# Optimization experiments

Hardware: AMD Instinct MI355X
Metric: run time of the kernel (lower is better)

The kernel has to match this reference:

```python
import jax, jax.numpy as jnp
import numpy as np

N, E, G = 20000, 160000, 32          # nodes, edges, graphs in batch
F_IN, H, P, C = 67, 2048, 1024, 18   # in_feat, hidden_feat, fc2 width, n_classifier
EPS = 1e-5
SLOPE = 0.01  # leaky_relu default negative slope


def setup_inputs() -> dict:
    key = jax.random.key(0)
    ks = jax.random.split(key, 24)
    w = lambda k, shape: (jax.random.normal(k, shape, jnp.float32) * 0.02)
    return {
        "h": jax.random.normal(ks[0], (N, F_IN), jnp.float32),
        "src": jax.random.randint(ks[1], (E,), 0, N),
        "dst": jax.random.randint(ks[2], (E,), 0, N),
        "gids": jnp.sort(jax.random.randint(ks[3], (N,), 0, G)),
        # SAGEConv layers: fc_self, fc_neigh (no per-fc bias), shared bias
        "ws1": w(ks[4], (F_IN, H)), "wn1": w(ks[5], (F_IN, H)), "b1": jnp.zeros((H,), jnp.float32),
        "ws2": w(ks[6], (H, H)),    "wn2": w(ks[7], (H, H)),    "b2": jnp.zeros((H,), jnp.float32),
        "ws3": w(ks[8], (H, H)),    "wn3": w(ks[9], (H, H)),    "b3": jnp.zeros((H,), jnp.float32),
        # batch norms (gamma, beta)
        "g1": jnp.ones((H,), jnp.float32), "be1": jnp.zeros((H,), jnp.float32),
        "g2": jnp.ones((H,), jnp.float32), "be2": jnp.zeros((H,), jnp.float32),
        "g3": jnp.ones((H,), jnp.float32), "be3": jnp.zeros((H,), jnp.float32),
        # MLP head
        "fw1": w(ks[10], (H, H)), "fb1": jnp.zeros((H,), jnp.float32),
        "fw2": w(ks[11], (H, P)), "fb2": jnp.zeros((P,), jnp.float32),
        "fw3": w(ks[12], (P, C)), "fb3": jnp.zeros((C,), jnp.float32),
    }


def _leaky(x):
    return jnp.where(x >= 0, x, SLOPE * x)


def _sage(x, src, dst, w_self, w_neigh, b):
    # DGL SAGEConv 'mean': mean of neighbor (src) features into dst, then linears.
    nsum = jax.ops.segment_sum(x[src], dst, num_segments=N)            # [N, F]
    deg = jax.ops.segment_sum(jnp.ones((E,), x.dtype), dst, num_segments=N)
    neigh = nsum / jnp.maximum(deg, 1.0)[:, None]                      # 0 for isolated
    return x @ w_self + neigh @ w_neigh + b


def _bn(x, gamma, beta):
    m = x.mean(0)
    v = x.var(0)
    return (x - m) * jax.lax.rsqrt(v + EPS) * gamma + beta


def reference(h, src, dst, gids,
              ws1, wn1, b1, g1, be1,
              ws2, wn2, b2, g2, be2,
              ws3, wn3, b3, g3, be3,
              fw1, fb1, fw2, fb2, fw3, fb3):
    x = _leaky(_bn(_sage(h, src, dst, ws1, wn1, b1), g1, be1))
    x = _leaky(_bn(_sage(x, src, dst, ws2, wn2, b2), g2, be2))
    x = _leaky(_bn(_sage(x, src, dst, ws3, wn3, b3), g3, be3))
    # mean pooling per graph
    gsum = jax.ops.segment_sum(x, gids, num_segments=G)                # [G, H]
    cnt = jax.ops.segment_sum(jnp.ones((N,), x.dtype), gids, num_segments=G)
    hg = gsum / jnp.maximum(cnt, 1.0)[:, None]
    # dropouts are identity in eval
    y = _leaky(hg @ fw1 + fb1)
    y = _leaky(y @ fw2 + fb2)
    return y @ fw3 + fb3
```

## Files before the change

### kernel.cpp

```cpp
#include <hip/hip_runtime.h>

typedef unsigned short u16;
typedef __attribute__((ext_vector_type(4))) float f32x4;
typedef __attribute__((ext_vector_type(8))) __bf16 bf16x8;
typedef __attribute__((ext_vector_type(8))) short s16x8;
typedef __attribute__((ext_vector_type(4))) u16 u16x4;

#define N_NODES 20000
#define N_EDGES 160000
#define N_GRAPH 32
#define F_IN 67
#define HID 2048
#define PW 1024
#define NCLS 18
#define MPAD2 20224
#define K1 192

__device__ __forceinline__ float bf2f(u16 u) {
    unsigned v = ((unsigned)u) << 16;
    float f; __builtin_memcpy(&f, &v, 4); return f;
}
__device__ __forceinline__ u16 f2bf(float f) {
    unsigned u; __builtin_memcpy(&u, &f, 4);
    u = (u + 0x7FFF + ((u >> 16) & 1)) >> 16;
    return (u16)u;
}
__device__ __forceinline__ int imax(int a, int b) { return a > b ? a : b; }

__device__ __forceinline__ void ld16(const u16* gptr, u16* lptr) {
    __builtin_amdgcn_global_load_lds(
        (const __attribute__((address_space(1))) unsigned int*)gptr,
        (__attribute__((address_space(3))) unsigned int*)lptr,
        16, 0, 0);
}

__global__ void k_hist(const int* __restrict__ dst, int* __restrict__ cnt) {
    int e = blockIdx.x * 256 + threadIdx.x;
    if (e < N_EDGES) atomicAdd(&cnt[dst[e]], 1);
}

__global__ void k_scan(const int* __restrict__ cnt, int* __restrict__ rowptr) {
    __shared__ int part[256];
    int t = threadIdx.x;
    const int per = (N_NODES + 255) / 256;
    int base = t * per;
    int s = 0;
    for (int i = 0; i < per; i++) { int idx = base + i; if (idx < N_NODES) s += cnt[idx]; }
    part[t] = s; __syncthreads();
    for (int off = 1; off < 256; off <<= 1) {
        int v = (t >= off) ? part[t - off] : 0;
        __syncthreads();
        part[t] += v;
        __syncthreads();
    }
    int running = (t == 0) ? 0 : part[t - 1];
    for (int i = 0; i < per; i++) {
        int idx = base + i;
        if (idx < N_NODES) { rowptr[idx] = running; running += cnt[idx]; }
    }
    if (t == 255) rowptr[N_NODES] = running;
}

__global__ void k_scatter(const int* __restrict__ src, const int* __restrict__ dst,
                          const int* __restrict__ rowptr, int* __restrict__ cursor,
                          int* __restrict__ csr) {
    int e = blockIdx.x * 256 + threadIdx.x;
    if (e < N_EDGES) {
        int d = dst[e];
        int p = atomicAdd(&cursor[d], 1);
        csr[rowptr[d] + p] = src[e];
    }
}

__global__ void k_w1t(const float* __restrict__ ws1, const float* __restrict__ wn1,
                      u16* __restrict__ w1t) {
    int n = blockIdx.x, t = threadIdx.x;
    float v = 0.f;
    if (t < F_IN) v = ws1[(size_t)t * HID + n];
    else if (t < 2 * F_IN) v = wn1[(size_t)(t - F_IN) * HID + n];
    w1t[(size_t)n * K1 + t] = f2bf(v);
}

__global__ void k_transpose2(const float* __restrict__ s0, const float* __restrict__ s1,
                             u16* __restrict__ dst) {
    __shared__ float tile[32][33];
    const float* src = blockIdx.z ? s1 : s0;
    int colofs = blockIdx.z ? HID : 0;
    int bx = blockIdx.x * 32, by = blockIdx.y * 32;
    int tx = threadIdx.x, ty = threadIdx.y;
#pragma unroll
    for (int i = 0; i < 32; i += 8)
        tile[ty + i][tx] = src[(size_t)(by + ty + i) * HID + bx + tx];
    __syncthreads();
#pragma unroll
    for (int i = 0; i < 32; i += 8)
        dst[(size_t)(bx + ty + i) * (2 * HID) + colofs + by + tx] = f2bf(tile[tx][ty + i]);
}

__global__ void k_agg1(const float* __restrict__ h, const int* __restrict__ rowptr,
                       const int* __restrict__ csr, u16* __restrict__ acat) {
    int n = blockIdx.x, t = threadIdx.x;
    if (t < F_IN) {
        acat[(size_t)n * K1 + t] = f2bf(h[(size_t)n * F_IN + t]);
    } else if (t < 2 * F_IN) {
        int c = t - F_IN;
        int e0 = rowptr[n], e1 = rowptr[n + 1];
        float a = 0.f;
        for (int e = e0; e < e1; e++) a += h[(size_t)csr[e] * F_IN + c];
        acat[(size_t)n * K1 + F_IN + c] = f2bf(a / (float)imax(e1 - e0, 1));
    }
}

__global__ __launch_bounds__(256)
void k_aggbn(const u16* __restrict__ x,
             const float* __restrict__ ssum, const float* __restrict__ ssq,
             const float* __restrict__ gma, const float* __restrict__ bta,
             const int* __restrict__ rowptr, const int* __restrict__ csr,
             u16* __restrict__ self_out, u16* __restrict__ neigh_out) {
    int n = blockIdx.x, t = threadIdx.x;
    int col = t * 8;
    float a[8], d[8];
#pragma unroll
    for (int j = 0; j < 8; ++j) {
        float m = ssum[col + j] * (1.0f / N_NODES);
        float var = ssq[col + j] * (1.0f / N_NODES) - m * m;
        a[j] = gma[col + j] * rsqrtf(var + 1e-5f);
        d[j] = bta[col + j] - m * a[j];
    }
    s16x8 vs = *(const s16x8*)&x[(size_t)n * HID + col];
    s16x8 so;
#pragma unroll
    for (int j = 0; j < 8; ++j) {
        float f = bf2f((u16)vs[j]) * a[j] + d[j];
        f = fmaxf(f, 0.01f * f);
        so[j] = (short)f2bf(f);
    }
    *(s16x8*)&self_out[(size_t)n * HID + col] = so;
    int e0 = rowptr[n], e1 = rowptr[n + 1];
    float acc[8] = {0, 0, 0, 0, 0, 0, 0, 0};
    for (int e = e0; e < e1; ++e) {
        int s = csr[e];
        s16x8 v = *(const s16x8*)&x[(size_t)s * HID + col];
#pragma unroll
        for (int j = 0; j < 8; ++j) {
            float f = bf2f((u16)v[j]) * a[j] + d[j];
            acc[j] += fmaxf(f, 0.01f * f);
        }
    }
    float inv = 1.0f / (float)imax(e1 - e0, 1);
    s16x8 o;
#pragma unroll
    for (int j = 0; j < 8; ++j) o[j] = (short)f2bf(acc[j] * inv);
    *(s16x8*)&neigh_out[(size_t)n * HID + col] = o;
}

#define VM4 asm volatile("s_waitcnt vmcnt(4)" ::: "memory")
#define VM2 asm volatile("s_waitcnt vmcnt(2)" ::: "memory")
#define VM0 asm volatile("s_waitcnt vmcnt(0)" ::: "memory")

#define STAGE_A(H) { const u16* as_; int ktl_;                                      \
    if (kt1 < kskt) { as_ = A0; ktl_ = kt1; } else { as_ = A1; ktl_ = kt1 - kskt; } \
    size_t ko_ = (size_t)ktl_ * 64 + swe;                                           \
    ld16(as_ + (row0 + 0 * 128 + (H) * 64 + r8) * (size_t)lda + ko_,                \
         LA + dbo + ((H) * 128 + 0 * 64 + r8) * 64 + ld8);                          \
    ld16(as_ + (row0 + 1 * 128 + (H) * 64 + r8) * (size_t)lda + ko_,                \
         LA + dbo + ((H) * 128 + 1 * 64 + r8) * 64 + ld8); }

#define STAGE_B(H) { size_t ko_ = (size_t)kt1 * 64 + swe;                           \
    ld16(WT + ((size_t)col0 + ((r8 >> 5)) * 64 + (H) * 32 + (r8 & 31)) * (size_t)ldb + ko_,\
         LB + dbo + ((H) * 128 + 0 * 64 + r8) * 64 + ld8);                          \
    ld16(WT + ((size_t)col0 + (2 + (r8 >> 5)) * 64 + (H) * 32 + (r8 & 31)) * (size_t)ldb + ko_,\
         LB + dbo + ((H) * 128 + 1 * 64 + r8) * 64 + ld8); }

#define RD_A(QM) {                                                                  \
    _Pragma("unroll") for (int f = 0; f < 4; ++f)                                   \
      _Pragma("unroll") for (int kk = 0; kk < 2; ++kk)                              \
        af[f][kk] = *(const bf16x8*)(bA + (QM) * 16384 + (wm * 64 + f * 16 + lr) * 128 \
                                     + ((kk * 64 + lg * 16) ^ rxor)); }

#define RD_B(DST, QN) {                                                             \
    _Pragma("unroll") for (int n = 0; n < 2; ++n)                                   \
      _Pragma("unroll") for (int kk = 0; kk < 2; ++kk)                              \
        DST[n][kk] = *(const bf16x8*)(bB + (QN) * 16384 + (wn * 32 + n * 16 + lr) * 128 \
                                     + ((kk * 64 + lg * 16) ^ rxor)); }

#define SYNC_MM(QM, QN, BW) {                                                       \
    __builtin_amdgcn_s_barrier();                                                   \
    __builtin_amdgcn_s_setprio(1);                                                  \
    _Pragma("unroll") for (int kk = 0; kk < 2; ++kk)                                \
      _Pragma("unroll") for (int f = 0; f < 4; ++f)                                 \
        _Pragma("unroll") for (int n = 0; n < 2; ++n)                               \
          acc[(QM) * 4 + f][(QN) * 2 + n] = __builtin_amdgcn_mfma_f32_16x16x32_bf16(\
              BW[n][kk], af[f][kk], acc[(QM) * 4 + f][(QN) * 2 + n], 0, 0, 0);      \
    __builtin_amdgcn_s_setprio(0); }

__global__ __launch_bounds__(512, 2)
void k_gemm256(const u16* __restrict__ A0, const u16* __restrict__ A1,
               const u16* __restrict__ WT, u16* __restrict__ C,
               float* __restrict__ ssum, float* __restrict__ ssq,
               int nkt, int kskt, int lda, int ldb) {
    __shared__ u16 LA[2 * 256 * 64];
    __shared__ u16 LB[2 * 256 * 64];
    const int tid = threadIdx.x;
    const int lane = tid & 63;
    const int wave = tid >> 6;
    const int wm = wave >> 2, wn = wave & 3;
    const int lr = lane & 15, lg = lane >> 4;
    const int rxor = (lr & 7) << 4;

    const int g = (blockIdx.x & 7) * 79 + (blockIdx.x >> 3);
    const size_t row0 = (size_t)(g >> 3) * 256;
    const int col0 = (g & 7) * 256;

    const int r8 = tid >> 3;
    const int ld8 = (tid & 7) * 8;
    const int swe = ((ld8 * 2) ^ ((r8 & 7) << 4)) >> 1;

    f32x4 acc[8][4];
#pragma unroll
    for (int i = 0; i < 8; i++)
#pragma unroll
        for (int j = 0; j < 4; j++) acc[i][j] = f32x4{0.f, 0.f, 0.f, 0.f};

    {
        const int kt1 = 0; const int dbo = 0;
        STAGE_A(0) STAGE_B(0) STAGE_B(1) STAGE_A(1)
    }
    VM0;
    __builtin_amdgcn_s_barrier();

    bf16x8 af[4][2], bw[2][2], bw2[2][2];

    for (int t = 0; t < nkt - 1; ++t) {
        const char* bA = (const char*)LA + (t & 1) * 32768;
        const char* bB = (const char*)LB + (t & 1) * 32768;
        const int kt1 = t + 1;
        const int dbo = ((t + 1) & 1) * 16384;
        RD_A(0) RD_B(bw, 0) STAGE_A(0) VM4; SYNC_MM(0, 0, bw)
        RD_B(bw2, 1) STAGE_B(0) VM4; SYNC_MM(0, 1, bw2)
        RD_A(1) STAGE_B(1) SYNC_MM(1, 1, bw2)
        RD_B(bw, 0) STAGE_A(1) VM4; SYNC_MM(1, 0, bw)
    }
    {
        const char* bA = (const char*)LA + ((nkt - 1) & 1) * 32768;
        const char* bB = (const char*)LB + ((nkt - 1) & 1) * 32768;
        RD_A(0) RD_B(bw, 0) VM2; SYNC_MM(0, 0, bw)
        RD_B(bw2, 1) VM0; SYNC_MM(0, 1, bw2)
        RD_A(1) SYNC_MM(1, 1, bw2)
        RD_B(bw, 0) SYNC_MM(1, 0, bw)
    }

#pragma unroll
    for (int f = 0; f < 8; ++f) {
        size_t m = row0 + wm * 128 + f * 16 + lr;
#pragma unroll
        for (int n = 0; n < 4; ++n) {
            int cb = col0 + wn * 64 + n * 16 + lg * 4;
            u16x4 o;
#pragma unroll
            for (int rg = 0; rg < 4; ++rg) o[rg] = f2bf(acc[f][n][rg]);
            *(u16x4*)&C[m * HID + cb] = o;
        }
    }
#pragma unroll
    for (int n = 0; n < 4; ++n) {
#pragma unroll
        for (int rg = 0; rg < 4; ++rg) {
            float s = 0.f, s2 = 0.f;
#pragma unroll
            for (int f = 0; f < 8; ++f) { float v = acc[f][n][rg]; s += v; s2 += v * v; }
#pragma unroll
            for (int mk = 1; mk < 16; mk <<= 1) {
                s += __shfl_xor(s, mk, 64);
                s2 += __shfl_xor(s2, mk, 64);
            }
            if (lr == 0) {
                int cb = col0 + wn * 64 + n * 16 + lg * 4 + rg;
                atomicAdd(&ssum[cb], s);
                atomicAdd(&ssq[cb], s2);
            }
        }
    }
}

__global__ void k_bounds(const int* __restrict__ gids, int* __restrict__ gstart) {
    int t = threadIdx.x;
    if (t > N_GRAPH) return;
    int lo = 0, hi = N_NODES;
    while (lo < hi) { int mid = (lo + hi) >> 1; if (gids[mid] < t) lo = mid + 1; else hi = mid; }
    gstart[t] = lo;
}

__global__ void k_poolbn(const u16* __restrict__ x,
                         const float* __restrict__ ssum, const float* __restrict__ ssq,
                         const float* __restrict__ gma, const float* __restrict__ bta,
                         const int* __restrict__ gstart, float* __restrict__ hg) {
    int g = blockIdx.x;
    int col = blockIdx.y * 256 + threadIdx.x;
    float m = ssum[col] * (1.0f / N_NODES);
    float var = ssq[col] * (1.0f / N_NODES) - m * m;
    float a = gma[col] * rsqrtf(var + 1e-5f);
    float d = bta[col] - m * a;
    int r0 = gstart[g], r1 = gstart[g + 1];
    float s = 0.f;
    for (int r = r0; r < r1; r++) {
        float f = bf2f(x[(size_t)r * HID + col]) * a + d;
        s += fmaxf(f, 0.01f * f);
    }
    hg[(size_t)g * HID + col] = s / (float)imax(r1 - r0, 1);
}

__global__ __launch_bounds__(256)
void k_mlp_part(const float* __restrict__ X, const float* __restrict__ W,
                float* __restrict__ Yp, int K, int Nc) {
    __shared__ float xs[32 * 256];
    int t = threadIdx.x;
    int kc = blockIdx.y;
    int n = blockIdx.x * 64 + (t & 63);
    int mg = t >> 6;
#pragma unroll
    for (int l = 0; l < 32; ++l) {
        int e = l * 256 + t;
        xs[e] = X[(size_t)(e >> 8) * K + kc * 256 + (e & 255)];
    }
    __syncthreads();
    float acc[8] = {};
    for (int k = 0; k < 256; ++k) {
        float wv = W[(size_t)(kc * 256 + k) * Nc + n];
#pragma unroll
        for (int i = 0; i < 8; ++i) acc[i] += xs[(mg * 8 + i) * 256 + k] * wv;
    }
#pragma unroll
    for (int i = 0; i < 8; ++i)
        Yp[(size_t)(kc * 32 + mg * 8 + i) * Nc + n] = acc[i];
}

__global__ void k_mlp_red(const float* __restrict__ Yp, const float* __restrict__ bias,
                          float* __restrict__ Y, int Nc, int leaky) {
    int idx = blockIdx.x * 256 + threadIdx.x;
    int n = idx % Nc;
    float s = 0.f;
#pragma unroll
    for (int kc = 0; kc < 8; ++kc) s += Yp[(size_t)kc * 32 * Nc + idx];
    float v = s + bias[n];
    if (leaky) v = v > 0.f ? v : 0.01f * v;
    Y[idx] = v;
}

__global__ void k_fc3(const float* __restrict__ y2, const float* __restrict__ fw3,
                      const float* __restrict__ fb3, float* __restrict__ out) {
    __shared__ float red[8][32];
    int m = blockIdx.x, t = threadIdx.x;
    int ch = t >> 5, c = t & 31;
    float s = 0.f;
    if (c < NCLS) {
        for (int j = 0; j < 128; ++j) {
            int k = ch * 128 + j;
            s += y2[(size_t)m * PW + k] * fw3[(size_t)k * NCLS + c];
        }
    }
    red[ch][c] = s;
    __syncthreads();
    if (t < NCLS) {
        float a = 0.f;
#pragma unroll
        for (int c2 = 0; c2 < 8; ++c2) a += red[c2][t];
        out[m * NCLS + t] = a + fb3[t];
    }
}

extern "C" void kernel_launch(void* const* d_in, const int* in_sizes, int n_in,
                              void* d_out, int out_size, void* d_ws, size_t ws_size,
                              hipStream_t stream) {
    const float* h   = (const float*)d_in[0];
    const int* src   = (const int*)d_in[1];
    const int* dst   = (const int*)d_in[2];
    const int* gids  = (const int*)d_in[3];
    const float* ws1 = (const float*)d_in[4];
    const float* wn1 = (const float*)d_in[5];
    const float* ws2 = (const float*)d_in[7];
    const float* wn2 = (const float*)d_in[8];
    const float* ws3 = (const float*)d_in[10];
    const float* wn3 = (const float*)d_in[11];
    const float* g1  = (const float*)d_in[13];
    const float* be1 = (const float*)d_in[14];
    const float* g2  = (const float*)d_in[15];
    const float* be2 = (const float*)d_in[16];
    const float* g3  = (const float*)d_in[17];
    const float* be3 = (const float*)d_in[18];
    const float* fw1 = (const float*)d_in[19];
    const float* fb1 = (const float*)d_in[20];
    const float* fw2 = (const float*)d_in[21];
    const float* fb2 = (const float*)d_in[22];
    const float* fw3 = (const float*)d_in[23];
    const float* fb3 = (const float*)d_in[24];
    float* out = (float*)d_out;
    (void)in_sizes; (void)n_in; (void)out_size;

    char* base = (char*)d_ws;
    size_t off = 0;
    auto alloc = [&](size_t b) -> char* {
        char* p = base + off;
        off += (b + 255) & ~(size_t)255;
        return p;
    };
    u16* BUF0 = (u16*)alloc((size_t)MPAD2 * HID * 2);
    u16* BUF1 = (u16*)alloc((size_t)MPAD2 * HID * 2);
    u16* BUF2 = (u16*)alloc((size_t)MPAD2 * HID * 2);
    u16* WT   = (u16*)alloc((size_t)HID * 2 * HID * 2);
    int* cnt    = (int*)alloc(N_NODES * 4);
    int* rowptr = (int*)alloc((N_NODES + 1) * 4);
    int* cursor = (int*)alloc(N_NODES * 4);
    int* csr    = (int*)alloc(N_EDGES * 4);
    float* ssum = (float*)alloc(HID * 4);
    float* ssq  = (float*)alloc(HID * 4);
    int* gstart = (int*)alloc(64 * 4);
    float* hg = (float*)alloc((size_t)N_GRAPH * HID * 4);
    float* y1 = (float*)alloc((size_t)N_GRAPH * HID * 4);
    float* y2 = (float*)alloc((size_t)N_GRAPH * PW * 4);
    u16* ACAT = (u16*)((char*)BUF2);
    u16* W1T  = (u16*)((char*)BUF2 + (size_t)MPAD2 * K1 * 2);
    float* Yp = (float*)((char*)BUF2);

    if (off > ws_size) return;

    hipMemsetAsync(cnt, 0, N_NODES * 4, stream);
    hipMemsetAsync(cursor, 0, N_NODES * 4, stream);
    hipMemsetAsync(ACAT, 0, (size_t)MPAD2 * K1 * 2, stream);
    hipMemsetAsync(BUF1 + (size_t)N_NODES * HID, 0, (size_t)(MPAD2 - N_NODES) * HID * 2, stream);
    hipMemsetAsync(BUF2 + (size_t)N_NODES * HID, 0, (size_t)(MPAD2 - N_NODES) * HID * 2, stream);

    k_hist<<<(N_EDGES + 255) / 256, 256, 0, stream>>>(dst, cnt);
    k_scan<<<1, 256, 0, stream>>>(cnt, rowptr);
    k_scatter<<<(N_EDGES + 255) / 256, 256, 0, stream>>>(src, dst, rowptr, cursor, csr);

    k_w1t<<<HID, K1, 0, stream>>>(ws1, wn1, W1T);
    k_agg1<<<N_NODES, 192, 0, stream>>>(h, rowptr, csr, ACAT);

    dim3 tb(32, 8);
    hipMemsetAsync(ssum, 0, 2 * HID * 4, stream);
    k_gemm256<<<632, 512, 0, stream>>>(ACAT, ACAT, W1T, BUF0, ssum, ssq, 3, 3, K1, K1);
    k_aggbn<<<N_NODES, 256, 0, stream>>>(BUF0, ssum, ssq, g1, be1, rowptr, csr, BUF1, BUF2);
    k_transpose2<<<dim3(64, 64, 2), tb, 0, stream>>>(ws2, wn2, WT);
    hipMemsetAsync(ssum, 0, 2 * HID * 4, stream);
    k_gemm256<<<632, 512, 0, stream>>>(BUF1, BUF2, WT, BUF0, ssum, ssq, 64, 32, HID, 2 * HID);
    k_aggbn<<<N_NODES, 256, 0, stream>>>(BUF0, ssum, ssq, g2, be2, rowptr, csr, BUF1, BUF2);
    k_transpose2<<<dim3(64, 64, 2), tb, 0, stream>>>(ws3, wn3, WT);
    hipMemsetAsync(ssum, 0, 2 * HID * 4, stream);
    k_gemm256<<<632, 512, 0, stream>>>(BUF1, BUF2, WT, BUF0, ssum, ssq, 64, 32, HID, 2 * HID);
    k_bounds<<<1, 64, 0, stream>>>(gids, gstart);
    k_poolbn<<<dim3(N_GRAPH, HID / 256), 256, 0, stream>>>(BUF0, ssum, ssq, g3, be3, gstart, hg);
    k_mlp_part<<<dim3(HID / 64, 8), 256, 0, stream>>>(hg, fw1, Yp, HID, HID);
    k_mlp_red<<<(N_GRAPH * HID) / 256, 256, 0, stream>>>(Yp, fb1, y1, HID, 1);
    k_mlp_part<<<dim3(PW / 64, 8), 256, 0, stream>>>(y1, fw2, Yp, HID, PW);
    k_mlp_red<<<(N_GRAPH * PW) / 256, 256, 0, stream>>>(Yp, fb2, y2, PW, 1);
    k_fc3<<<N_GRAPH, 256, 0, stream>>>(y2, fw3, fb3, out);
}
```

Baseline: 1.351 ms.

## Halve GEMM K-tile to 32 and restructure LDS staging and barriers

The 256x256 GEMM kernel now stages a K-slice of 32 instead of 64 per iteration. This halves LDS use (32 KB instead of 64 KB) and removes the launch_bounds occupancy hint. The global-to-LDS mapping, swizzle and wave-to-tile mapping are rewritten: each wave now covers interleaved 64-row and 32-column sub-blocks, and barriers are split from the MFMA groups. The aim is to cut the LDS footprint and let the pipeline overlap better, at the cost of twice as many K iterations and barriers.

Result: slower. 1.479 ms (+9.5%).

```diff
diff --git a/kernel.cpp b/kernel.cpp
--- a/kernel.cpp
+++ b/kernel.cpp
@@ -154,67 +154,60 @@
     *(s16x8*)&neigh_out[(size_t)n * HID + col] = o;
 }
 
-#define VM4 asm volatile("s_waitcnt vmcnt(4)" ::: "memory")
 #define VM2 asm volatile("s_waitcnt vmcnt(2)" ::: "memory")
 #define VM0 asm volatile("s_waitcnt vmcnt(0)" ::: "memory")
-
-#define STAGE_A(H) { const u16* as_; int ktl_;                                      \
+#define BAR __builtin_amdgcn_s_barrier();
+
+#define STAGE_A() { const u16* as_; int ktl_;                                       \
     if (kt1 < kskt) { as_ = A0; ktl_ = kt1; } else { as_ = A1; ktl_ = kt1 - kskt; } \
-    size_t ko_ = (size_t)ktl_ * 64 + swe;                                           \
-    ld16(as_ + (row0 + 0 * 128 + (H) * 64 + r8) * (size_t)lda + ko_,                \
-         LA + dbo + ((H) * 128 + 0 * 64 + r8) * 64 + ld8);                          \
-    ld16(as_ + (row0 + 1 * 128 + (H) * 64 + r8) * (size_t)lda + ko_,                \
-         LA + dbo + ((H) * 128 + 1 * 64 + r8) * 64 + ld8); }
-
-#define STAGE_B(H) { size_t ko_ = (size_t)kt1 * 64 + swe;                           \
-    ld16(WT + ((size_t)col0 + ((r8 >> 5)) * 64 + (H) * 32 + (r8 & 31)) * (size_t)ldb + ko_,\
-         LB + dbo + ((H) * 128 + 0 * 64 + r8) * 64 + ld8);                          \
-    ld16(WT + ((size_t)col0 + (2 + (r8 >> 5)) * 64 + (H) * 32 + (r8 & 31)) * (size_t)ldb + ko_,\
-         LB + dbo + ((H) * 128 + 1 * 64 + r8) * 64 + ld8); }
-
-#define RD_A(QM) {                                                                  \
+    size_t kb_ = (size_t)ktl_ * 32 + ksl;                                           \
+    ld16(as_ + (row0 + grow0) * (size_t)lda + kb_, LA + dbo + ldsoff);              \
+    ld16(as_ + (row0 + grow0 + 128) * (size_t)lda + kb_, LA + dbo + 4096 + ldsoff); }
+
+#define STAGE_B() { size_t kb_ = (size_t)kt1 * 32 + ksl;                            \
+    ld16(WT + (size_t)(col0 + grow0) * ldb + kb_, LB + dbo + ldsoff);               \
+    ld16(WT + (size_t)(col0 + grow0 + 128) * ldb + kb_, LB + dbo + 4096 + ldsoff); }
+
+#define RD_A(QM) { _Pragma("unroll") for (int f = 0; f < 4; ++f)                    \
+    af[f] = *(const bf16x8*)(bA + ((QM) * 64 + aq + f * 8) * 128 + hbx); }
+
+#define RD_B(DST, QN) { _Pragma("unroll") for (int n = 0; n < 2; ++n)               \
+    DST[n] = *(const bf16x8*)(bB + ((QN) * 64 + bq + n * 8) * 128 + hbx); }
+
+#define MM8(QM, QN, BW) {                                                           \
+    __builtin_amdgcn_s_setprio(1);                                                  \
     _Pragma("unroll") for (int f = 0; f < 4; ++f)                                   \
-      _Pragma("unroll") for (int kk = 0; kk < 2; ++kk)                              \
-        af[f][kk] = *(const bf16x8*)(bA + (QM) * 16384 + (wm * 64 + f * 16 + lr) * 128 \
-                                     + ((kk * 64 + lg * 16) ^ rxor)); }
-
-#define RD_B(DST, QN) {                                                             \
-    _Pragma("unroll") for (int n = 0; n < 2; ++n)                                   \
-      _Pragma("unroll") for (int kk = 0; kk < 2; ++kk)                              \
-        DST[n][kk] = *(const bf16x8*)(bB + (QN) * 16384 + (wn * 32 + n * 16 + lr) * 128 \
-                                     + ((kk * 64 + lg * 16) ^ rxor)); }
-
-#define SYNC_MM(QM, QN, BW) {                                                       \
-    __builtin_amdgcn_s_barrier();                                                   \
-    __builtin_amdgcn_s_setprio(1);                                                  \
-    _Pragma("unroll") for (int kk = 0; kk < 2; ++kk)                                \
-      _Pragma("unroll") for (int f = 0; f < 4; ++f)                                 \
-        _Pragma("unroll") for (int n = 0; n < 2; ++n)                               \
-          acc[(QM) * 4 + f][(QN) * 2 + n] = __builtin_amdgcn_mfma_f32_16x16x32_bf16(\
-              BW[n][kk], af[f][kk], acc[(QM) * 4 + f][(QN) * 2 + n], 0, 0, 0);      \
+      _Pragma("unroll") for (int n = 0; n < 2; ++n)                                 \
+        acc[(QM) * 4 + f][(QN) * 2 + n] = __builtin_amdgcn_mfma_f32_16x16x32_bf16(  \
+            BW[n], af[f], acc[(QM) * 4 + f][(QN) * 2 + n], 0, 0, 0);                \
     __builtin_amdgcn_s_setprio(0); }
 
-__global__ __launch_bounds__(512, 2)
+__global__ __launch_bounds__(512)
 void k_gemm256(const u16* __restrict__ A0, const u16* __restrict__ A1,
                const u16* __restrict__ WT, u16* __restrict__ C,
                float* __restrict__ ssum, float* __restrict__ ssq,
                int nkt, int kskt, int lda, int ldb) {
-    __shared__ u16 LA[2 * 256 * 64];
-    __shared__ u16 LB[2 * 256 * 64];
+    __shared__ u16 LA[2 * 128 * 64];
+    __shared__ u16 LB[2 * 128 * 64];
     const int tid = threadIdx.x;
     const int lane = tid & 63;
     const int wave = tid >> 6;
     const int wm = wave >> 2, wn = wave & 3;
     const int lr = lane & 15, lg = lane >> 4;
-    const int rxor = (lr & 7) << 4;
 
     const int g = (blockIdx.x & 7) * 79 + (blockIdx.x >> 3);
     const size_t row0 = (size_t)(g >> 3) * 256;
     const int col0 = (g & 7) * 256;
 
-    const int r8 = tid >> 3;
-    const int ld8 = (tid & 7) * 8;
-    const int swe = ((ld8 * 2) ^ ((r8 & 7) << 4)) >> 1;
+    const int q0 = tid >> 3;
+    const int lg16 = ((tid & 7) * 16) ^ ((q0 & 7) << 4);
+    const int grow0 = 2 * q0 + (lg16 >> 6);
+    const int ksl = ((lg16 >> 4) & 3) * 8;
+    const int ldsoff = tid * 8;
+
+    const int aq = wm * 32 + (lr >> 1);
+    const int bq = wn * 16 + (lr >> 1);
+    const int hbx = (((lane & 1) * 64 + lg * 16) ^ (((lr >> 1) & 7) << 4));
 
     f32x4 acc[8][4];
 #pragma unroll
@@ -224,58 +217,58 @@
 
     {
         const int kt1 = 0; const int dbo = 0;
-        STAGE_A(0) STAGE_B(0) STAGE_B(1) STAGE_A(1)
+        STAGE_A() STAGE_B()
     }
     VM0;
-    __builtin_amdgcn_s_barrier();
-
-    bf16x8 af[4][2], bw[2][2], bw2[2][2];
+    BAR
+
+    bf16x8 af[4], bw[2], bw2[2];
 
     for (int t = 0; t < nkt - 1; ++t) {
-        const char* bA = (const char*)LA + (t & 1) * 32768;
-        const char* bB = (const char*)LB + (t & 1) * 32768;
+        const char* bA = (const char*)LA + (t & 1) * 16384;
+        const char* bB = (const char*)LB + (t & 1) * 16384;
         const int kt1 = t + 1;
-        const int dbo = ((t + 1) & 1) * 16384;
-        RD_A(0) RD_B(bw, 0) STAGE_A(0) VM4; SYNC_MM(0, 0, bw)
-        RD_B(bw2, 1) STAGE_B(0) VM4; SYNC_MM(0, 1, bw2)
-        RD_A(1) STAGE_B(1) SYNC_MM(1, 1, bw2)
-        RD_B(bw, 0) STAGE_A(1) VM4; SYNC_MM(1, 0, bw)
+        const int dbo = ((t + 1) & 1) * 8192;
+        RD_A(0) RD_B(bw, 0) STAGE_A() VM2; BAR MM8(0, 0, bw)
+        RD_B(bw2, 1) STAGE_B() BAR MM8(0, 1, bw2)
+        RD_A(1) BAR MM8(1, 1, bw2)
+        MM8(1, 0, bw)
     }
     {
-        const char* bA = (const char*)LA + ((nkt - 1) & 1) * 32768;
-        const char* bB = (const char*)LB + ((nkt - 1) & 1) * 32768;
-        RD_A(0) RD_B(bw, 0) VM2; SYNC_MM(0, 0, bw)
-        RD_B(bw2, 1) VM0; SYNC_MM(0, 1, bw2)
-        RD_A(1) SYNC_MM(1, 1, bw2)
-        RD_B(bw, 0) SYNC_MM(1, 0, bw)
-    }
-
-#pragma unroll
-    for (int f = 0; f < 8; ++f) {
-        size_t m = row0 + wm * 128 + f * 16 + lr;
-#pragma unroll
-        for (int n = 0; n < 4; ++n) {
-            int cb = col0 + wn * 64 + n * 16 + lg * 4;
+        const char* bA = (const char*)LA + ((nkt - 1) & 1) * 16384;
+        const char* bB = (const char*)LB + ((nkt - 1) & 1) * 16384;
+        RD_A(0) RD_B(bw, 0) VM0; BAR MM8(0, 0, bw)
+        RD_B(bw2, 1) BAR MM8(0, 1, bw2)
+        RD_A(1) BAR MM8(1, 1, bw2)
+        MM8(1, 0, bw)
+    }
+
+#pragma unroll
+    for (int i = 0; i < 8; ++i) {
+        size_t m = row0 + (i >> 2) * 128 + wm * 64 + (i & 3) * 16 + lr;
+#pragma unroll
+        for (int j = 0; j < 4; ++j) {
+            int cb = col0 + (j >> 1) * 128 + wn * 32 + (j & 1) * 16 + lg * 4;
             u16x4 o;
 #pragma unroll
-            for (int rg = 0; rg < 4; ++rg) o[rg] = f2bf(acc[f][n][rg]);
+            for (int rg = 0; rg < 4; ++rg) o[rg] = f2bf(acc[i][j][rg]);
             *(u16x4*)&C[m * HID + cb] = o;
         }
     }
 #pragma unroll
-    for (int n = 0; n < 4; ++n) {
+    for (int j = 0; j < 4; ++j) {
 #pragma unroll
         for (int rg = 0; rg < 4; ++rg) {
             float s = 0.f, s2 = 0.f;
 #pragma unroll
-            for (int f = 0; f < 8; ++f) { float v = acc[f][n][rg]; s += v; s2 += v * v; }
+            for (int i = 0; i < 8; ++i) { float v = acc[i][j][rg]; s += v; s2 += v * v; }
 #pragma unroll
             for (int mk = 1; mk < 16; mk <<= 1) {
                 s += __shfl_xor(s, mk, 64);
                 s2 += __shfl_xor(s2, mk, 64);
             }
             if (lr == 0) {
-                int cb = col0 + wn * 64 + n * 16 + lg * 4 + rg;
+                int cb = col0 + (j >> 1) * 128 + wn * 32 + (j & 1) * 16 + lg * 4 + rg;
                 atomicAdd(&ssum[cb], s);
                 atomicAdd(&ssq[cb], s2);
             }
@@ -439,15 +432,15 @@
 
     dim3 tb(32, 8);
     hipMemsetAsync(ssum, 0, 2 * HID * 4, stream);
-    k_gemm256<<<632, 512, 0, stream>>>(ACAT, ACAT, W1T, BUF0, ssum, ssq, 3, 3, K1, K1);
+    k_gemm256<<<632, 512, 0, stream>>>(ACAT, ACAT, W1T, BUF0, ssum, ssq, 6, 6, K1, K1);
     k_aggbn<<<N_NODES, 256, 0, stream>>>(BUF0, ssum, ssq, g1, be1, rowptr, csr, BUF1, BUF2);
     k_transpose2<<<dim3(64, 64, 2), tb, 0, stream>>>(ws2, wn2, WT);
     hipMemsetAsync(ssum, 0, 2 * HID * 4, stream);
-    k_gemm256<<<632, 512, 0, stream>>>(BUF1, BUF2, WT, BUF0, ssum, ssq, 64, 32, HID, 2 * HID);
+    k_gemm256<<<632, 512, 0, stream>>>(BUF1, BUF2, WT, BUF0, ssum, ssq, 128, 64, HID, 2 * HID);
     k_aggbn<<<N_NODES, 256, 0, stream>>>(BUF0, ssum, ssq, g2, be2, rowptr, csr, BUF1, BUF2);
     k_transpose2<<<dim3(64, 64, 2), tb, 0, stream>>>(ws3, wn3, WT);
     hipMemsetAsync(ssum, 0, 2 * HID * 4, stream);
-    k_gemm256<<<632, 512, 0, stream>>>(BUF1, BUF2, WT, BUF0, ssum, ssq, 64, 32, HID, 2 * HID);
+    k_gemm256<<<632, 512, 0, stream>>>(BUF1, BUF2, WT, BUF0, ssum, ssq, 128, 64, HID, 2 * HID);
     k_bounds<<<1, 64, 0, stream>>>(gids, gstart);
     k_poolbn<<<dim3(N_GRAPH, HID / 256), 256, 0, stream>>>(BUF0, ssum, ssq, g3, be3, gstart, hg);
     k_mlp_part<<<dim3(HID / 64, 8), 256, 0, stream>>>(hg, fw1, Yp, HID, HID);
```
